# Performance work log

Measured on AMD Instinct MI355X. Metric: run time of the kernel, lower is better.

Reference implementation:

```python
import jax, jax.numpy as jnp
import numpy as np


def setup_inputs() -> dict:
    key = jax.random.key(0)
    features = jax.random.normal(key, (8192, 128), dtype=jnp.float32)
    return {"features": features}


def reference(features):
    # Pairwise negative L2 distance: -||f_i - f_j||_2, computed via the
    # squared-norm + GEMM identity to avoid the O(N^2*D) broadcast intermediate:
    #   ||f_i - f_j||^2 = ||f_i||^2 + ||f_j||^2 - 2 f_i . f_j
    sq = jnp.sum(features * features, axis=-1)          # [N]
    gram = features @ features.T                         # [N, N]
    d2 = sq[:, None] + sq[None, :] - 2.0 * gram          # [N, N]
    d2 = jnp.maximum(d2, 0.0)                            # clamp fp roundoff
    return -jnp.sqrt(d2)
```

## Files before the change

### kernel.cpp

```cpp
#include <hip/hip_runtime.h>
#include <hip/hip_bf16.h>

typedef __attribute__((ext_vector_type(8))) short short8;
typedef __attribute__((ext_vector_type(4))) float float4v;

#define N_PTS 8192
#define DIM   128
#define BM    128

__device__ __forceinline__ unsigned short f2bf(float f) {
    unsigned u = __builtin_bit_cast(unsigned, f);
    u += 0x7fffu + ((u >> 16) & 1u);
    return (unsigned short)(u >> 16);
}
__device__ __forceinline__ float bf2f(unsigned short h) {
    unsigned u = ((unsigned)h) << 16;
    return __builtin_bit_cast(float, u);
}

__global__ __launch_bounds__(256, 2)
void fsim_kernel(const float* __restrict__ F, float* __restrict__ out) {
    __shared__ short As[BM * DIM];
    __shared__ short Bs[BM * DIM];

    const int t    = threadIdx.x;
    const int brow = blockIdx.y;
    const int bcol = blockIdx.x;

    const int r    = t & 127;
    const int isB  = t >> 7;
    const int grow = (isB ? bcol : brow) * BM + r;
    const float* __restrict__ src = F + (size_t)grow * DIM;
    short* dst = isB ? Bs : As;
    float s = 0.f;
#pragma unroll
    for (int i = 0; i < 16; ++i) {
        float4v f0 = *(const float4v*)(src + i * 8);
        float4v f1 = *(const float4v*)(src + i * 8 + 4);
        short8 p;
#pragma unroll
        for (int k = 0; k < 4; ++k) {
            unsigned short b0 = f2bf(f0[k]);
            unsigned short b1 = f2bf(f1[k]);
            p[k]     = (short)b0;
            p[k + 4] = (short)b1;
            float v0 = bf2f(b0), v1 = bf2f(b1);
            s += v0 * v0 + v1 * v1;
        }
        const int pg = (i ^ (r & 15)) * 8;
        *(short8*)(dst + r * DIM + pg) = p;
    }
    __syncthreads();

    const int lane = t & 63;
    const int w    = t >> 6;
    const int wr   = (w >> 1) * 64;
    const int wc   = (w & 1) * 64;
    const int lrow = lane & 15;
    const int quad = lane >> 4;

    float4v acc[4][4];
#pragma unroll
    for (int a = 0; a < 4; ++a)
#pragma unroll
        for (int b = 0; b < 4; ++b)
            acc[a][b] = (float4v){0.f, 0.f, 0.f, 0.f};

#pragma unroll
    for (int ks = 0; ks < 4; ++ks) {
        short8 af[4], bfv[4];
        const int g = ks * 4 + quad;
#pragma unroll
        for (int mt = 0; mt < 4; ++mt) {
            const int row = wr + mt * 16 + lrow;
            af[mt] = *(const short8*)(As + row * DIM + ((g ^ (row & 15)) * 8));
        }
#pragma unroll
        for (int nt = 0; nt < 4; ++nt) {
            const int row = wc + nt * 16 + lrow;
            bfv[nt] = *(const short8*)(Bs + row * DIM + ((g ^ (row & 15)) * 8));
        }
#pragma unroll
        for (int mt = 0; mt < 4; ++mt)
#pragma unroll
            for (int nt = 0; nt < 4; ++nt)
                acc[mt][nt] = __builtin_amdgcn_mfma_f32_16x16x32_bf16(
                    af[mt], bfv[nt], acc[mt][nt], 0, 0, 0);
    }

    __syncthreads();
    float* sqf = (float*)As;
    sqf[t] = s;
    __syncthreads();

    const size_t orow0    = (size_t)brow * BM;
    const int    col_base = bcol * BM;
#pragma unroll
    for (int mt = 0; mt < 4; ++mt) {
#pragma unroll
        for (int nt = 0; nt < 4; ++nt) {
            const int n   = wc + nt * 16 + lrow;
            const float sc = sqf[128 + n];
            const int col = col_base + n;
#pragma unroll
            for (int reg = 0; reg < 4; ++reg) {
                const int m  = wr + mt * 16 + quad * 4 + reg;
                const float sr = sqf[m];
                float d2 = sr + sc - 2.0f * acc[mt][nt][reg];
                d2 = d2 > 0.f ? d2 : 0.f;
                out[(orow0 + m) * (size_t)N_PTS + col] = -__builtin_sqrtf(d2);
            }
        }
    }
}

extern "C" void kernel_launch(void* const* d_in, const int* in_sizes, int n_in,
                              void* d_out, int out_size, void* d_ws, size_t ws_size,
                              hipStream_t stream) {
    const float* F = (const float*)d_in[0];
    float* out = (float*)d_out;
    dim3 grid(N_PTS / BM, N_PTS / BM);
    fsim_kernel<<<grid, 256, 0, stream>>>(F, out);
}
```

Before: 304.4 us.

## Precompute bf16 features and norms in a prep kernel, load tiles via global_load_lds

Result: faster. 273.1 us (-10.3%).

```diff
diff --git a/kernel.cpp b/kernel.cpp
--- a/kernel.cpp
+++ b/kernel.cpp
@@ -7,6 +7,9 @@
 #define N_PTS 8192
 #define DIM   128
 #define BM    128
+
+typedef const __attribute__((address_space(1))) void* gptr_t;
+typedef __attribute__((address_space(3))) void* lptr_t;
 
 __device__ __forceinline__ unsigned short f2bf(float f) {
     unsigned u = __builtin_bit_cast(unsigned, f);
@@ -18,25 +21,18 @@
     return __builtin_bit_cast(float, u);
 }
 
-__global__ __launch_bounds__(256, 2)
-void fsim_kernel(const float* __restrict__ F, float* __restrict__ out) {
-    __shared__ short As[BM * DIM];
-    __shared__ short Bs[BM * DIM];
-
-    const int t    = threadIdx.x;
-    const int brow = blockIdx.y;
-    const int bcol = blockIdx.x;
-
-    const int r    = t & 127;
-    const int isB  = t >> 7;
-    const int grow = (isB ? bcol : brow) * BM + r;
-    const float* __restrict__ src = F + (size_t)grow * DIM;
-    short* dst = isB ? Bs : As;
+__global__ __launch_bounds__(128)
+void prep_kernel(const float* __restrict__ F,
+                 unsigned short* __restrict__ bfF,
+                 float* __restrict__ sqg) {
+    const int row = blockIdx.x * 128 + threadIdx.x;
+    const float* __restrict__ src = F + (size_t)row * DIM;
+    unsigned short* dst = bfF + (size_t)row * DIM;
     float s = 0.f;
 #pragma unroll
-    for (int i = 0; i < 16; ++i) {
-        float4v f0 = *(const float4v*)(src + i * 8);
-        float4v f1 = *(const float4v*)(src + i * 8 + 4);
+    for (int g = 0; g < 16; ++g) {
+        float4v f0 = *(const float4v*)(src + g * 8);
+        float4v f1 = *(const float4v*)(src + g * 8 + 4);
         short8 p;
 #pragma unroll
         for (int k = 0; k < 4; ++k) {
@@ -47,13 +43,42 @@
             float v0 = bf2f(b0), v1 = bf2f(b1);
             s += v0 * v0 + v1 * v1;
         }
-        const int pg = (i ^ (r & 15)) * 8;
-        *(short8*)(dst + r * DIM + pg) = p;
+        *(short8*)(dst + (g ^ (row & 15)) * 8) = p;
     }
+    sqg[row] = s;
+}
+
+__global__ __launch_bounds__(256, 2)
+void fsim_kernel(const unsigned short* __restrict__ bfF,
+                 const float* __restrict__ sqg,
+                 float* __restrict__ out) {
+    __shared__ unsigned short As[BM * DIM];
+    __shared__ unsigned short Bs[BM * DIM];
+    __shared__ float sqA[BM];
+    __shared__ float sqB[BM];
+
+    const int t    = threadIdx.x;
+    const int lane = t & 63;
+    const int w    = t >> 6;
+    const int brow = blockIdx.y;
+    const int bcol = blockIdx.x;
+
+    const char* gA = (const char*)(bfF + (size_t)brow * BM * DIM);
+    const char* gB = (const char*)(bfF + (size_t)bcol * BM * DIM);
+    char* lA = (char*)As;
+    char* lB = (char*)Bs;
+    const int off = w * 8192 + lane * 16;
+#pragma unroll
+    for (int i = 0; i < 8; ++i) {
+        __builtin_amdgcn_global_load_lds((gptr_t)(gA + off + i * 1024),
+                                         (lptr_t)(lA + off + i * 1024), 16, 0, 0);
+        __builtin_amdgcn_global_load_lds((gptr_t)(gB + off + i * 1024),
+                                         (lptr_t)(lB + off + i * 1024), 16, 0, 0);
+    }
+    if (t < 128) sqA[t] = sqg[brow * BM + t];
+    else         sqB[t - 128] = sqg[bcol * BM + (t - 128)];
     __syncthreads();
 
-    const int lane = t & 63;
-    const int w    = t >> 6;
     const int wr   = (w >> 1) * 64;
     const int wc   = (w & 1) * 64;
     const int lrow = lane & 15;
@@ -73,12 +98,12 @@
 #pragma unroll
         for (int mt = 0; mt < 4; ++mt) {
             const int row = wr + mt * 16 + lrow;
-            af[mt] = *(const short8*)(As + row * DIM + ((g ^ (row & 15)) * 8));
+            af[mt] = *(const short8*)((const short*)As + row * DIM + ((g ^ (row & 15)) * 8));
         }
 #pragma unroll
         for (int nt = 0; nt < 4; ++nt) {
             const int row = wc + nt * 16 + lrow;
-            bfv[nt] = *(const short8*)(Bs + row * DIM + ((g ^ (row & 15)) * 8));
+            bfv[nt] = *(const short8*)((const short*)Bs + row * DIM + ((g ^ (row & 15)) * 8));
         }
 #pragma unroll
         for (int mt = 0; mt < 4; ++mt)
@@ -88,27 +113,24 @@
                     af[mt], bfv[nt], acc[mt][nt], 0, 0, 0);
     }
 
-    __syncthreads();
-    float* sqf = (float*)As;
-    sqf[t] = s;
-    __syncthreads();
-
     const size_t orow0    = (size_t)brow * BM;
     const int    col_base = bcol * BM;
+    float scb[4];
+#pragma unroll
+    for (int nt = 0; nt < 4; ++nt) scb[nt] = sqB[wc + nt * 16 + lrow];
 #pragma unroll
     for (int mt = 0; mt < 4; ++mt) {
 #pragma unroll
-        for (int nt = 0; nt < 4; ++nt) {
-            const int n   = wc + nt * 16 + lrow;
-            const float sc = sqf[128 + n];
-            const int col = col_base + n;
+        for (int reg = 0; reg < 4; ++reg) {
+            const int m  = wr + mt * 16 + quad * 4 + reg;
+            const float sr = sqA[m];
+            float* orow = out + (orow0 + m) * (size_t)N_PTS + col_base;
 #pragma unroll
-            for (int reg = 0; reg < 4; ++reg) {
-                const int m  = wr + mt * 16 + quad * 4 + reg;
-                const float sr = sqf[m];
-                float d2 = sr + sc - 2.0f * acc[mt][nt][reg];
+            for (int nt = 0; nt < 4; ++nt) {
+                const int n = wc + nt * 16 + lrow;
+                float d2 = sr + scb[nt] - 2.0f * acc[mt][nt][reg];
                 d2 = d2 > 0.f ? d2 : 0.f;
-                out[(orow0 + m) * (size_t)N_PTS + col] = -__builtin_sqrtf(d2);
+                orow[n] = -__builtin_sqrtf(d2);
             }
         }
     }
@@ -119,6 +141,10 @@
                               hipStream_t stream) {
     const float* F = (const float*)d_in[0];
     float* out = (float*)d_out;
+    unsigned short* bfF = (unsigned short*)d_ws;
+    float* sqg = (float*)((char*)d_ws + (size_t)N_PTS * DIM * 2);
+
+    prep_kernel<<<dim3(N_PTS / 128), 128, 0, stream>>>(F, bfF, sqg);
     dim3 grid(N_PTS / BM, N_PTS / BM);
-    fsim_kernel<<<grid, 256, 0, stream>>>(F, out);
+    fsim_kernel<<<grid, 256, 0, stream>>>(bfF, sqg, out);
 }
```
